# Performance work log

Measured on AMD Instinct MI355X. Metric: run time of the kernel, lower is better.

## Reference

```python
import jax, jax.numpy as jnp
import numpy as np

B, C, H, W = 32, 256, 8, 8
N = H * W                      # n_objects = 64
D_G_IN = 2 * C + 2             # pair concat + 2-dim relative position = 514
HG = 512                       # g hidden / output dim
HF = 512                       # f hidden dim
D_OUT = 256                    # f output dim


def _relative_grid_feat():
    # feat[p, q, 0] = oh(p) - oh(q); feat[p, q, 1] = ow(p) - ow(q); zero-centered globally
    idx = jnp.arange(N)
    oh, ow = idx // W, idx % W
    r0 = (oh[:, None] - oh[None, :]).astype(jnp.float32)
    r1 = (ow[:, None] - ow[None, :]).astype(jnp.float32)
    rel = jnp.stack([r0, r1], axis=-1)  # [N, N, 2]
    return rel - rel.mean()


def setup_inputs() -> dict:
    key = jax.random.key(0)
    ks = jax.random.split(key, 11)
    s = 0.02
    return {
        "x": jax.random.normal(ks[0], (B, C, H, W), dtype=jnp.float32),
        "g_W0": jax.random.normal(ks[1], (D_G_IN, HG), dtype=jnp.float32) * s,
        "g_b0": jnp.zeros((HG,), dtype=jnp.float32),
        "g_W1": jax.random.normal(ks[2], (HG, HG), dtype=jnp.float32) * s,
        "g_b1": jnp.zeros((HG,), dtype=jnp.float32),
        "g_W2": jax.random.normal(ks[3], (HG, HG), dtype=jnp.float32) * s,
        "g_b2": jnp.zeros((HG,), dtype=jnp.float32),
        "f_W0": jax.random.normal(ks[4], (HG, HF), dtype=jnp.float32) * s,
        "f_b0": jnp.zeros((HF,), dtype=jnp.float32),
        "f_W1": jax.random.normal(ks[5], (HF, D_OUT), dtype=jnp.float32) * s,
        "f_b1": jnp.zeros((D_OUT,), dtype=jnp.float32),
    }


def reference(x, g_W0, g_b0, g_W1, g_b1, g_W2, g_b2, f_W0, f_b0, f_W1, f_b1):
    relu = jax.nn.relu
    x_flat = x.reshape(B, C, N)                     # [B, C, N]
    xT = jnp.transpose(x_flat, (0, 2, 1))           # [B, N, C]
    # pair index k = p*N + q: xi takes object q (inner), xj takes object p (outer)
    xi = jnp.broadcast_to(xT[:, None, :, :], (B, N, N, C))
    xj = jnp.broadcast_to(xT[:, :, None, :], (B, N, N, C))
    rel = jnp.broadcast_to(_relative_grid_feat()[None], (B, N, N, 2))
    pair = jnp.concatenate([xi, xj, rel], axis=-1)  # [B, N, N, 2C+2]
    # g MLP (nonlinear=True -> activation on output too)
    h = relu(jnp.einsum('bpqd,dh->bpqh', pair, g_W0) + g_b0)
    h = relu(jnp.einsum('bpqh,hk->bpqk', h, g_W1) + g_b1)
    relations = relu(jnp.einsum('bpqh,hk->bpqk', h, g_W2) + g_b2)  # [B, N, N, HG]
    embedding = relations.sum(axis=(1, 2))          # sum over all pairs -> [B, HG]
    # f MLP (linear output)
    hf = relu(embedding @ f_W0 + f_b0)
    out = hf @ f_W1 + f_b1                          # [B, D_OUT]
    return out
```

## Files before the change

kernel.cpp:

```cpp
#include <hip/hip_runtime.h>


typedef short short8 __attribute__((ext_vector_type(8)));
typedef float f32x16 __attribute__((ext_vector_type(16)));

__device__ __forceinline__ unsigned short f2bf(float f) {
    unsigned u = __builtin_bit_cast(unsigned, f);
    u = (u + 0x7FFFu + ((u >> 16) & 1u)) >> 16;
    return (unsigned short)u;
}

__device__ __forceinline__ unsigned cvt_pk(float a, float b) {
    unsigned r;
    asm("v_cvt_pk_bf16_f32 %0, %1, %2" : "=v"(r) : "v"(a), "v"(b));
    return r;
}

__global__ __launch_bounds__(512) void uv_kernel(
    const float* __restrict__ x, const float* __restrict__ W0,
    const float* __restrict__ b0, float* __restrict__ Up, float* __restrict__ Vp)
{
    __shared__ float xs[256 * 8];
    const int blk = blockIdx.x;
    const int b = blk >> 3, n0 = (blk & 7) * 8;
    const int tid = threadIdx.x;

    for (int i = tid; i < 2048; i += 512) {
        int c = i >> 3, r = i & 7;
        xs[i] = x[((size_t)b * 256 + c) * 64 + n0 + r];
    }
    __syncthreads();

    const int h = tid;
    float ua[8], va[8];
#pragma unroll
    for (int r = 0; r < 8; ++r) { ua[r] = 0.f; va[r] = 0.f; }

#pragma unroll 4
    for (int c = 0; c < 256; ++c) {
        float wa = W0[(size_t)c * 512 + h];
        float wb = W0[(size_t)(256 + c) * 512 + h];
#pragma unroll
        for (int r = 0; r < 8; ++r) {
            float xv = xs[c * 8 + r];
            ua[r] += xv * wa;
            va[r] += xv * wb;
        }
    }
    const float w2a = W0[(size_t)512 * 512 + h];
    const float w2b = W0[(size_t)513 * 512 + h];
    const float bb = b0[h];
#pragma unroll
    for (int r = 0; r < 8; ++r) {
        int n = n0 + r;
        float fh = (float)(n >> 3), fw = (float)(n & 7);
        Up[((size_t)b * 64 + n) * 512 + h] = ua[r] - fh * w2a - fw * w2b;
        Vp[((size_t)b * 64 + n) * 512 + h] = va[r] + fh * w2a + fw * w2b + bb;
    }
}

__global__ __launch_bounds__(256) void wswz_kernel(
    const float* __restrict__ W1, const float* __restrict__ W2,
    unsigned short* __restrict__ W1s, unsigned short* __restrict__ W2s,
    float* __restrict__ emb)
{
    int gid = blockIdx.x * 256 + threadIdx.x;
    if (gid < 16384) emb[gid] = 0.f;
    int m = gid >> 15;
    int idx = gid & 32767;
    int col = idx & 511;
    int kg = idx >> 9;
    const float* W = m ? W2 : W1;
    unsigned short* O = m ? W2s : W1s;
    short8 v;
#pragma unroll
    for (int j = 0; j < 8; ++j)
        v[j] = (short)f2bf(W[(size_t)(kg * 8 + j) * 512 + col]);
    *(short8*)(O + (size_t)idx * 8) = v;
}

__global__ __launch_bounds__(1024, 4) void main_kernel(
    const float* __restrict__ Up, const float* __restrict__ Vp,
    const unsigned short* __restrict__ W1s, const unsigned short* __restrict__ W2s,
    const float* __restrict__ b1, const float* __restrict__ b2,
    float* __restrict__ emb)
{
    extern __shared__ __align__(16) unsigned char lds[];

    const int wg = ((blockIdx.x & 7) << 7) | (blockIdx.x >> 3);
    const int b = wg >> 5, pp = wg & 31;

    const int tid = threadIdx.x;
    const int lane = tid & 63, wave = tid >> 6;
    const int l31 = lane & 31, lg = lane >> 5;
    const int swz = (l31 & 15) << 4;
    const int t = wave & 1;
    const int wcol = (wave >> 1) << 6;
    unsigned char* T = lds + t * 65536;

    {
        const int bt = tid >> 9;
        const int cc = tid & 63;
        const int r0 = (tid >> 6) & 7;
        const int p = pp * 2 + bt;
        unsigned char* TB = lds + bt * 65536;
        float4 u0[8], u1[8];
#pragma unroll
        for (int it = 0; it < 8; ++it) {
            const float* ub = Up + ((size_t)(b * 64 + r0 + it * 8)) * 512 + cc * 8;
            u0[it] = *(const float4*)(ub);
            u1[it] = *(const float4*)(ub + 4);
        }
        const float* vp = Vp + ((size_t)(b * 64 + p)) * 512 + cc * 8;
        float4 v0 = *(const float4*)(vp), v1 = *(const float4*)(vp + 4);
#pragma unroll
        for (int it = 0; it < 8; ++it) {
            int row = r0 + it * 8;
            int off = row * 1024 + ((cc * 16) ^ ((row & 15) << 4));
            uint4 w;
            w.x = cvt_pk(fmaxf(u0[it].x + v0.x, 0.f), fmaxf(u0[it].y + v0.y, 0.f));
            w.y = cvt_pk(fmaxf(u0[it].z + v0.z, 0.f), fmaxf(u0[it].w + v0.w, 0.f));
            w.z = cvt_pk(fmaxf(u1[it].x + v1.x, 0.f), fmaxf(u1[it].y + v1.y, 0.f));
            w.w = cvt_pk(fmaxf(u1[it].z + v1.z, 0.f), fmaxf(u1[it].w + v1.w, 0.f));
            *(uint4*)(&TB[off]) = w;
        }
    }
    __syncthreads();

    const int arow0 = l31 * 1024;
    const int arow1 = (l31 + 32) * 1024;

    f32x16 acc[2][2];
#pragma unroll
    for (int i = 0; i < 2; ++i)
#pragma unroll
        for (int j = 0; j < 2; ++j) acc[i][j] = (f32x16)0.f;

    {
        const unsigned short* wb = W1s + ((size_t)(lg * 512 + wcol + l31)) * 8;
        short8 wn0 = *(const short8*)(wb);
        short8 wn1 = *(const short8*)(wb + 256);
        __builtin_amdgcn_s_setprio(1);
#pragma unroll
        for (int ks = 0; ks < 32; ++ks) {
            short8 cw0 = wn0, cw1 = wn1;
            if (ks < 31) {
                const unsigned short* np = wb + (size_t)(ks + 1) * 8192;
                wn0 = *(const short8*)(np);
                wn1 = *(const short8*)(np + 256);
            }
            int achunk = (ks * 32 + lg * 16) ^ swz;
            short8 a0 = *(const short8*)(&T[arow0 + achunk]);
            short8 a1 = *(const short8*)(&T[arow1 + achunk]);
            acc[0][0] = __builtin_amdgcn_mfma_f32_32x32x16_bf16(cw0, a0, acc[0][0], 0, 0, 0);
            acc[1][0] = __builtin_amdgcn_mfma_f32_32x32x16_bf16(cw1, a0, acc[1][0], 0, 0, 0);
            acc[0][1] = __builtin_amdgcn_mfma_f32_32x32x16_bf16(cw0, a1, acc[0][1], 0, 0, 0);
            acc[1][1] = __builtin_amdgcn_mfma_f32_32x32x16_bf16(cw1, a1, acc[1][1], 0, 0, 0);
        }
        __builtin_amdgcn_s_setprio(0);
    }
    __syncthreads();

    {
#pragma unroll
        for (int hf = 0; hf < 2; ++hf) {
#pragma unroll
            for (int g = 0; g < 4; ++g) {
                int h = wcol + hf * 32 + g * 8 + 4 * lg;
                float4 bb = *(const float4*)(b1 + h);
#pragma unroll
                for (int qf = 0; qf < 2; ++qf) {
                    int q = qf * 32 + l31;
                    float a0 = fmaxf(acc[hf][qf][g * 4 + 0] + bb.x, 0.f);
                    float a1 = fmaxf(acc[hf][qf][g * 4 + 1] + bb.y, 0.f);
                    float a2 = fmaxf(acc[hf][qf][g * 4 + 2] + bb.z, 0.f);
                    float a3 = fmaxf(acc[hf][qf][g * 4 + 3] + bb.w, 0.f);
                    uint2 pk;
                    pk.x = cvt_pk(a0, a1);
                    pk.y = cvt_pk(a2, a3);
                    int off = q * 1024 + ((h * 2) ^ ((q & 15) << 4));
                    *(uint2*)(&T[off]) = pk;
                }
            }
        }
    }
    __syncthreads();

    f32x16 acc2[2][2];
#pragma unroll
    for (int i = 0; i < 2; ++i)
#pragma unroll
        for (int j = 0; j < 2; ++j) acc2[i][j] = (f32x16)0.f;

    {
        const unsigned short* wb = W2s + ((size_t)(lg * 512 + wcol + l31)) * 8;
        short8 wn0 = *(const short8*)(wb);
        short8 wn1 = *(const short8*)(wb + 256);
        __builtin_amdgcn_s_setprio(1);
#pragma unroll
        for (int ks = 0; ks < 32; ++ks) {
            short8 cw0 = wn0, cw1 = wn1;
            if (ks < 31) {
                const unsigned short* np = wb + (size_t)(ks + 1) * 8192;
                wn0 = *(const short8*)(np);
                wn1 = *(const short8*)(np + 256);
            }
            int achunk = (ks * 32 + lg * 16) ^ swz;
            short8 a0 = *(const short8*)(&T[arow0 + achunk]);
            short8 a1 = *(const short8*)(&T[arow1 + achunk]);
            acc2[0][0] = __builtin_amdgcn_mfma_f32_32x32x16_bf16(a0, cw0, acc2[0][0], 0, 0, 0);
            acc2[1][0] = __builtin_amdgcn_mfma_f32_32x32x16_bf16(a1, cw0, acc2[1][0], 0, 0, 0);
            acc2[0][1] = __builtin_amdgcn_mfma_f32_32x32x16_bf16(a0, cw1, acc2[0][1], 0, 0, 0);
            acc2[1][1] = __builtin_amdgcn_mfma_f32_32x32x16_bf16(a1, cw1, acc2[1][1], 0, 0, 0);
        }
        __builtin_amdgcn_s_setprio(0);
    }

    {
        float s[2];
#pragma unroll
        for (int cf = 0; cf < 2; ++cf) {
            int col = wcol + cf * 32 + l31;
            float bias = b2[col];
            float tt = 0.f;
#pragma unroll
            for (int qf = 0; qf < 2; ++qf)
#pragma unroll
                for (int reg = 0; reg < 16; ++reg)
                    tt += fmaxf(acc2[qf][cf][reg] + bias, 0.f);
            tt += __shfl_xor(tt, 32);
            s[cf] = tt;
        }
        if (lane < 32) {
            unsafeAtomicAdd(&emb[b * 512 + wcol + lane], s[0]);
            unsafeAtomicAdd(&emb[b * 512 + wcol + 32 + lane], s[1]);
        }
    }
}

__global__ __launch_bounds__(256) void f0_kernel(
    const float* __restrict__ emb, const float* __restrict__ fW0,
    const float* __restrict__ fb0, float* __restrict__ hs)
{
    __shared__ float es[512];
    __shared__ float red[256];
    const int b = blockIdx.x >> 3, s = blockIdx.x & 7;
    const int t = threadIdx.x;
    const int colL = t & 63, cg = t >> 6;
    es[t] = emb[b * 512 + t];
    es[t + 256] = emb[b * 512 + 256 + t];
    __syncthreads();
    const int col = s * 64 + colL;
    float a = 0.f;
    const int c0 = cg * 128;
#pragma unroll 4
    for (int c = c0; c < c0 + 128; ++c)
        a += es[c] * fW0[(size_t)c * 512 + col];
    red[t] = a;
    __syncthreads();
    if (t < 64) {
        float r = red[t] + red[t + 64] + red[t + 128] + red[t + 192] + fb0[col];
        hs[b * 512 + col] = fmaxf(r, 0.f);
    }
}

__global__ __launch_bounds__(256) void f1_kernel(
    const float* __restrict__ hs, const float* __restrict__ fW1,
    const float* __restrict__ fb1, float* __restrict__ out)
{
    __shared__ float es[512];
    __shared__ float red[256];
    const int b = blockIdx.x >> 2, s = blockIdx.x & 3;
    const int t = threadIdx.x;
    const int colL = t & 63, cg = t >> 6;
    es[t] = hs[b * 512 + t];
    es[t + 256] = hs[b * 512 + 256 + t];
    __syncthreads();
    const int col = s * 64 + colL;
    float a = 0.f;
    const int c0 = cg * 128;
#pragma unroll 4
    for (int c = c0; c < c0 + 128; ++c)
        a += es[c] * fW1[(size_t)c * 256 + col];
    red[t] = a;
    __syncthreads();
    if (t < 64) {
        out[b * 256 + col] = red[t] + red[t + 64] + red[t + 128] + red[t + 192] + fb1[col];
    }
}

extern "C" void kernel_launch(void* const* d_in, const int* in_sizes, int n_in,
                              void* d_out, int out_size, void* d_ws, size_t ws_size,
                              hipStream_t stream)
{
    const float* x   = (const float*)d_in[0];
    const float* gW0 = (const float*)d_in[1];
    const float* gb0 = (const float*)d_in[2];
    const float* gW1 = (const float*)d_in[3];
    const float* gb1 = (const float*)d_in[4];
    const float* gW2 = (const float*)d_in[5];
    const float* gb2 = (const float*)d_in[6];
    const float* fW0 = (const float*)d_in[7];
    const float* fb0 = (const float*)d_in[8];
    const float* fW1 = (const float*)d_in[9];
    const float* fb1 = (const float*)d_in[10];
    float* out = (float*)d_out;

    char* ws = (char*)d_ws;
    float* Up           = (float*)(ws);
    float* Vp           = (float*)(ws + (4 << 20));
    unsigned short* W1s = (unsigned short*)(ws + (8 << 20));
    unsigned short* W2s = (unsigned short*)(ws + (8 << 20) + (512 << 10));
    float* emb          = (float*)(ws + (9 << 20));
    float* hs           = (float*)(ws + (9 << 20) + (64 << 10));

    uv_kernel<<<256, 512, 0, stream>>>(x, gW0, gb0, Up, Vp);
    wswz_kernel<<<256, 256, 0, stream>>>(gW1, gW2, W1s, W2s, emb);
    main_kernel<<<1024, 1024, 131072, stream>>>(Up, Vp, W1s, W2s, gb1, gb2, emb);
    f0_kernel<<<256, 256, 0, stream>>>(emb, fW0, fb0, hs);
    f1_kernel<<<128, 256, 0, stream>>>(hs, fW1, fb1, out);
}
```

Measured before the change: 185.5 us.

## Halve main kernel waves with wider per-wave tiles, merge prep kernels

The main kernel drops from 1024 to 512 threads. Each wave now computes a 128-column slice with four weight fragments per k-step, doubling the accumulators so each LDS A-fragment and weight load feeds more MFMAs. The LDS swizzle moves to 8-byte granularity, with A fragments read as two uint2 loads. The uv and weight-swizzle kernels are merged into one launch to save a kernel launch. The cost is higher register pressure (eight f32x16 accumulators per wave) and fewer waves to hide memory latency.

```diff
diff --git a/kernel.cpp b/kernel.cpp
--- a/kernel.cpp
+++ b/kernel.cpp
@@ -16,14 +16,45 @@
     return r;
 }
 
-__global__ __launch_bounds__(512) void uv_kernel(
+__device__ __forceinline__ short8 lds_frag(const unsigned char* T, int row, int chunk) {
+    const int base = row * 1024;
+    const int s = (row & 15) << 3;
+    uint2 lo = *(const uint2*)(T + base + (chunk ^ s));
+    uint2 hi = *(const uint2*)(T + base + ((chunk + 8) ^ s));
+    uint4 u; u.x = lo.x; u.y = lo.y; u.z = hi.x; u.w = hi.y;
+    return __builtin_bit_cast(short8, u);
+}
+
+__global__ __launch_bounds__(512) void pre_kernel(
     const float* __restrict__ x, const float* __restrict__ W0,
-    const float* __restrict__ b0, float* __restrict__ Up, float* __restrict__ Vp)
+    const float* __restrict__ b0,
+    const float* __restrict__ W1, const float* __restrict__ W2,
+    float* __restrict__ Up, float* __restrict__ Vp,
+    unsigned short* __restrict__ W1s, unsigned short* __restrict__ W2s,
+    float* __restrict__ emb)
 {
     __shared__ float xs[256 * 8];
+    const int tid = threadIdx.x;
+
+    if (blockIdx.x >= 256) {
+        int gid = (blockIdx.x - 256) * 512 + tid;
+        if (gid < 16384) emb[gid] = 0.f;
+        int m = gid >> 15;
+        int idx = gid & 32767;
+        int col = idx & 511;
+        int kg = idx >> 9;
+        const float* W = m ? W2 : W1;
+        unsigned short* O = m ? W2s : W1s;
+        short8 v;
+#pragma unroll
+        for (int j = 0; j < 8; ++j)
+            v[j] = (short)f2bf(W[(size_t)(kg * 8 + j) * 512 + col]);
+        *(short8*)(O + (size_t)idx * 8) = v;
+        return;
+    }
+
     const int blk = blockIdx.x;
     const int b = blk >> 3, n0 = (blk & 7) * 8;
-    const int tid = threadIdx.x;
 
     for (int i = tid; i < 2048; i += 512) {
         int c = i >> 3, r = i & 7;
@@ -59,51 +90,30 @@
     }
 }
 
-__global__ __launch_bounds__(256) void wswz_kernel(
-    const float* __restrict__ W1, const float* __restrict__ W2,
-    unsigned short* __restrict__ W1s, unsigned short* __restrict__ W2s,
-    float* __restrict__ emb)
-{
-    int gid = blockIdx.x * 256 + threadIdx.x;
-    if (gid < 16384) emb[gid] = 0.f;
-    int m = gid >> 15;
-    int idx = gid & 32767;
-    int col = idx & 511;
-    int kg = idx >> 9;
-    const float* W = m ? W2 : W1;
-    unsigned short* O = m ? W2s : W1s;
-    short8 v;
-#pragma unroll
-    for (int j = 0; j < 8; ++j)
-        v[j] = (short)f2bf(W[(size_t)(kg * 8 + j) * 512 + col]);
-    *(short8*)(O + (size_t)idx * 8) = v;
-}
-
-__global__ __launch_bounds__(1024, 4) void main_kernel(
+__global__ __launch_bounds__(512, 2) void main_kernel(
     const float* __restrict__ Up, const float* __restrict__ Vp,
     const unsigned short* __restrict__ W1s, const unsigned short* __restrict__ W2s,
     const float* __restrict__ b1, const float* __restrict__ b2,
     float* __restrict__ emb)
 {
     extern __shared__ __align__(16) unsigned char lds[];
+    unsigned char* T0 = lds;
+    unsigned char* T1 = lds + 65536;
 
     const int wg = ((blockIdx.x & 7) << 7) | (blockIdx.x >> 3);
     const int b = wg >> 5, pp = wg & 31;
+    const int p0 = pp * 2, p1 = p0 + 1;
 
     const int tid = threadIdx.x;
     const int lane = tid & 63, wave = tid >> 6;
     const int l31 = lane & 31, lg = lane >> 5;
-    const int swz = (l31 & 15) << 4;
     const int t = wave & 1;
-    const int wcol = (wave >> 1) << 6;
-    unsigned char* T = lds + t * 65536;
-
-    {
-        const int bt = tid >> 9;
+    const int wcol = (wave >> 1) << 7;
+    unsigned char* T = t ? T1 : T0;
+
+    {
         const int cc = tid & 63;
-        const int r0 = (tid >> 6) & 7;
-        const int p = pp * 2 + bt;
-        unsigned char* TB = lds + bt * 65536;
+        const int r0 = tid >> 6;
         float4 u0[8], u1[8];
 #pragma unroll
         for (int it = 0; it < 8; ++it) {
@@ -111,28 +121,36 @@
             u0[it] = *(const float4*)(ub);
             u1[it] = *(const float4*)(ub + 4);
         }
-        const float* vp = Vp + ((size_t)(b * 64 + p)) * 512 + cc * 8;
-        float4 v0 = *(const float4*)(vp), v1 = *(const float4*)(vp + 4);
+        const float* vA = Vp + ((size_t)(b * 64 + p0)) * 512 + cc * 8;
+        const float* vB = Vp + ((size_t)(b * 64 + p1)) * 512 + cc * 8;
+        float4 vA0 = *(const float4*)(vA), vA1 = *(const float4*)(vA + 4);
+        float4 vB0 = *(const float4*)(vB), vB1 = *(const float4*)(vB + 4);
 #pragma unroll
         for (int it = 0; it < 8; ++it) {
             int row = r0 + it * 8;
-            int off = row * 1024 + ((cc * 16) ^ ((row & 15) << 4));
-            uint4 w;
-            w.x = cvt_pk(fmaxf(u0[it].x + v0.x, 0.f), fmaxf(u0[it].y + v0.y, 0.f));
-            w.y = cvt_pk(fmaxf(u0[it].z + v0.z, 0.f), fmaxf(u0[it].w + v0.w, 0.f));
-            w.z = cvt_pk(fmaxf(u1[it].x + v1.x, 0.f), fmaxf(u1[it].y + v1.y, 0.f));
-            w.w = cvt_pk(fmaxf(u1[it].z + v1.z, 0.f), fmaxf(u1[it].w + v1.w, 0.f));
-            *(uint4*)(&TB[off]) = w;
-        }
-    }
-    __syncthreads();
-
-    const int arow0 = l31 * 1024;
-    const int arow1 = (l31 + 32) * 1024;
-
-    f32x16 acc[2][2];
-#pragma unroll
-    for (int i = 0; i < 2; ++i)
+            int base = row * 1024;
+            int s = (row & 15) << 3;
+            int x = cc * 16;
+            uint2 wlo, whi;
+            wlo.x = cvt_pk(fmaxf(u0[it].x + vA0.x, 0.f), fmaxf(u0[it].y + vA0.y, 0.f));
+            wlo.y = cvt_pk(fmaxf(u0[it].z + vA0.z, 0.f), fmaxf(u0[it].w + vA0.w, 0.f));
+            whi.x = cvt_pk(fmaxf(u1[it].x + vA1.x, 0.f), fmaxf(u1[it].y + vA1.y, 0.f));
+            whi.y = cvt_pk(fmaxf(u1[it].z + vA1.z, 0.f), fmaxf(u1[it].w + vA1.w, 0.f));
+            *(uint2*)(&T0[base + (x ^ s)]) = wlo;
+            *(uint2*)(&T0[base + ((x + 8) ^ s)]) = whi;
+            wlo.x = cvt_pk(fmaxf(u0[it].x + vB0.x, 0.f), fmaxf(u0[it].y + vB0.y, 0.f));
+            wlo.y = cvt_pk(fmaxf(u0[it].z + vB0.z, 0.f), fmaxf(u0[it].w + vB0.w, 0.f));
+            whi.x = cvt_pk(fmaxf(u1[it].x + vB1.x, 0.f), fmaxf(u1[it].y + vB1.y, 0.f));
+            whi.y = cvt_pk(fmaxf(u1[it].z + vB1.z, 0.f), fmaxf(u1[it].w + vB1.w, 0.f));
+            *(uint2*)(&T1[base + (x ^ s)]) = wlo;
+            *(uint2*)(&T1[base + ((x + 8) ^ s)]) = whi;
+        }
+    }
+    __syncthreads();
+
+    f32x16 acc[4][2];
+#pragma unroll
+    for (int i = 0; i < 4; ++i)
 #pragma unroll
         for (int j = 0; j < 2; ++j) acc[i][j] = (f32x16)0.f;
 
@@ -140,22 +158,30 @@
         const unsigned short* wb = W1s + ((size_t)(lg * 512 + wcol + l31)) * 8;
         short8 wn0 = *(const short8*)(wb);
         short8 wn1 = *(const short8*)(wb + 256);
+        short8 wn2 = *(const short8*)(wb + 512);
+        short8 wn3 = *(const short8*)(wb + 768);
         __builtin_amdgcn_s_setprio(1);
 #pragma unroll
         for (int ks = 0; ks < 32; ++ks) {
-            short8 cw0 = wn0, cw1 = wn1;
+            short8 cw0 = wn0, cw1 = wn1, cw2 = wn2, cw3 = wn3;
             if (ks < 31) {
                 const unsigned short* np = wb + (size_t)(ks + 1) * 8192;
                 wn0 = *(const short8*)(np);
                 wn1 = *(const short8*)(np + 256);
+                wn2 = *(const short8*)(np + 512);
+                wn3 = *(const short8*)(np + 768);
             }
-            int achunk = (ks * 32 + lg * 16) ^ swz;
-            short8 a0 = *(const short8*)(&T[arow0 + achunk]);
-            short8 a1 = *(const short8*)(&T[arow1 + achunk]);
+            int chunk = ks * 32 + lg * 16;
+            short8 a0 = lds_frag(T, l31, chunk);
+            short8 a1 = lds_frag(T, l31 + 32, chunk);
             acc[0][0] = __builtin_amdgcn_mfma_f32_32x32x16_bf16(cw0, a0, acc[0][0], 0, 0, 0);
             acc[1][0] = __builtin_amdgcn_mfma_f32_32x32x16_bf16(cw1, a0, acc[1][0], 0, 0, 0);
+            acc[2][0] = __builtin_amdgcn_mfma_f32_32x32x16_bf16(cw2, a0, acc[2][0], 0, 0, 0);
+            acc[3][0] = __builtin_amdgcn_mfma_f32_32x32x16_bf16(cw3, a0, acc[3][0], 0, 0, 0);
             acc[0][1] = __builtin_amdgcn_mfma_f32_32x32x16_bf16(cw0, a1, acc[0][1], 0, 0, 0);
             acc[1][1] = __builtin_amdgcn_mfma_f32_32x32x16_bf16(cw1, a1, acc[1][1], 0, 0, 0);
+            acc[2][1] = __builtin_amdgcn_mfma_f32_32x32x16_bf16(cw2, a1, acc[2][1], 0, 0, 0);
+            acc[3][1] = __builtin_amdgcn_mfma_f32_32x32x16_bf16(cw3, a1, acc[3][1], 0, 0, 0);
         }
         __builtin_amdgcn_s_setprio(0);
     }
@@ -163,7 +189,7 @@
 
     {
 #pragma unroll
-        for (int hf = 0; hf < 2; ++hf) {
+        for (int hf = 0; hf < 4; ++hf) {
 #pragma unroll
             for (int g = 0; g < 4; ++g) {
                 int h = wcol + hf * 32 + g * 8 + 4 * lg;
@@ -178,7 +204,7 @@
                     uint2 pk;
                     pk.x = cvt_pk(a0, a1);
                     pk.y = cvt_pk(a2, a3);
-                    int off = q * 1024 + ((h * 2) ^ ((q & 15) << 4));
+                    int off = q * 1024 + ((h * 2) ^ ((q & 15) << 3));
                     *(uint2*)(&T[off]) = pk;
                 }
             }
@@ -186,40 +212,47 @@
     }
     __syncthreads();
 
-    f32x16 acc2[2][2];
+    f32x16 acc2[2][4];
 #pragma unroll
     for (int i = 0; i < 2; ++i)
 #pragma unroll
-        for (int j = 0; j < 2; ++j) acc2[i][j] = (f32x16)0.f;
+        for (int j = 0; j < 4; ++j) acc2[i][j] = (f32x16)0.f;
 
     {
         const unsigned short* wb = W2s + ((size_t)(lg * 512 + wcol + l31)) * 8;
         short8 wn0 = *(const short8*)(wb);
         short8 wn1 = *(const short8*)(wb + 256);
+        short8 wn2 = *(const short8*)(wb + 512);
+        short8 wn3 = *(const short8*)(wb + 768);
         __builtin_amdgcn_s_setprio(1);
 #pragma unroll
         for (int ks = 0; ks < 32; ++ks) {
-            short8 cw0 = wn0, cw1 = wn1;
+            short8 cw0 = wn0, cw1 = wn1, cw2 = wn2, cw3 = wn3;
             if (ks < 31) {
                 const unsigned short* np = wb + (size_t)(ks + 1) * 8192;
                 wn0 = *(const short8*)(np);
                 wn1 = *(const short8*)(np + 256);
+                wn2 = *(const short8*)(np + 512);
+                wn3 = *(const short8*)(np + 768);
             }
-            int achunk = (ks * 32 + lg * 16) ^ swz;
-            short8 a0 = *(const short8*)(&T[arow0 + achunk]);
-            short8 a1 = *(const short8*)(&T[arow1 + achunk]);
+            int chunk = ks * 32 + lg * 16;
+            short8 a0 = lds_frag(T, l31, chunk);
+            short8 a1 = lds_frag(T, l31 + 32, chunk);
             acc2[0][0] = __builtin_amdgcn_mfma_f32_32x32x16_bf16(a0, cw0, acc2[0][0], 0, 0, 0);
             acc2[1][0] = __builtin_amdgcn_mfma_f32_32x32x16_bf16(a1, cw0, acc2[1][0], 0, 0, 0);
             acc2[0][1] = __builtin_amdgcn_mfma_f32_32x32x16_bf16(a0, cw1, acc2[0][1], 0, 0, 0);
             acc2[1][1] = __builtin_amdgcn_mfma_f32_32x32x16_bf16(a1, cw1, acc2[1][1], 0, 0, 0);
+            acc2[0][2] = __builtin_amdgcn_mfma_f32_32x32x16_bf16(a0, cw2, acc2[0][2], 0, 0, 0);
+            acc2[1][2] = __builtin_amdgcn_mfma_f32_32x32x16_bf16(a1, cw2, acc2[1][2], 0, 0, 0);
+            acc2[0][3] = __builtin_amdgcn_mfma_f32_32x32x16_bf16(a0, cw3, acc2[0][3], 0, 0, 0);
+            acc2[1][3] = __builtin_amdgcn_mfma_f32_32x32x16_bf16(a1, cw3, acc2[1][3], 0, 0, 0);
         }
         __builtin_amdgcn_s_setprio(0);
     }
 
     {
-        float s[2];
-#pragma unroll
-        for (int cf = 0; cf < 2; ++cf) {
+#pragma unroll
+        for (int cf = 0; cf < 4; ++cf) {
             int col = wcol + cf * 32 + l31;
             float bias = b2[col];
             float tt = 0.f;
@@ -229,11 +262,8 @@
                 for (int reg = 0; reg < 16; ++reg)
                     tt += fmaxf(acc2[qf][cf][reg] + bias, 0.f);
             tt += __shfl_xor(tt, 32);
-            s[cf] = tt;
-        }
-        if (lane < 32) {
-            unsafeAtomicAdd(&emb[b * 512 + wcol + lane], s[0]);
-            unsafeAtomicAdd(&emb[b * 512 + wcol + 32 + lane], s[1]);
+            if (lane < 32)
+                unsafeAtomicAdd(&emb[b * 512 + col], tt);
         }
     }
 }
@@ -314,9 +344,8 @@
     float* emb          = (float*)(ws + (9 << 20));
     float* hs           = (float*)(ws + (9 << 20) + (64 << 10));
 
-    uv_kernel<<<256, 512, 0, stream>>>(x, gW0, gb0, Up, Vp);
-    wswz_kernel<<<256, 256, 0, stream>>>(gW1, gW2, W1s, W2s, emb);
-    main_kernel<<<1024, 1024, 131072, stream>>>(Up, Vp, W1s, W2s, gb1, gb2, emb);
+    pre_kernel<<<384, 512, 0, stream>>>(x, gW0, gb0, gW1, gW2, Up, Vp, W1s, W2s, emb);
+    main_kernel<<<1024, 512, 131072, stream>>>(Up, Vp, W1s, W2s, gb1, gb2, emb);
     f0_kernel<<<256, 256, 0, stream>>>(emb, fW0, fb0, hs);
     f1_kernel<<<128, 256, 0, stream>>>(hs, fW1, fb1, out);
 }
```

After: 190.4 us. 1.03x slower.
